# Performance work log

Hardware: AMD Instinct MI355X
Metric: run time of the kernel (lower is better)

The kernel has to match this reference:

```python
import jax, jax.numpy as jnp
import numpy as np

EMBED_DIM = 768
NUM_HEADS = 12
D_K = EMBED_DIM // NUM_HEADS


def setup_inputs() -> dict:
    key = jax.random.key(0)
    ks = jax.random.split(key, 9)
    b, s, d = 4, 2048, EMBED_DIM
    scale = 1.0 / np.sqrt(d)
    x = jax.random.normal(ks[0], (b, s, d), dtype=jnp.float32)
    return {
        "x": x,
        "w_q": jax.random.normal(ks[1], (d, d), dtype=jnp.float32) * scale,
        "b_q": jnp.zeros((d,), dtype=jnp.float32),
        "w_k": jax.random.normal(ks[2], (d, d), dtype=jnp.float32) * scale,
        "b_k": jnp.zeros((d,), dtype=jnp.float32),
        "w_v": jax.random.normal(ks[3], (d, d), dtype=jnp.float32) * scale,
        "b_v": jnp.zeros((d,), dtype=jnp.float32),
        "w_o": jax.random.normal(ks[4], (d, d), dtype=jnp.float32) * scale,
        "b_o": jnp.zeros((d,), dtype=jnp.float32),
    }


def reference(x, w_q, b_q, w_k, b_k, w_v, b_v, w_o, b_o):
    b, s, d = x.shape
    h, dk = NUM_HEADS, D_K
    # projections (torch Linear: x @ W^T + b)
    q = (x @ w_q.T + b_q).reshape(b, s, h, dk).transpose(0, 2, 1, 3)
    k = (x @ w_k.T + b_k).reshape(b, s, h, dk).transpose(0, 2, 1, 3)
    v = (x @ w_v.T + b_v).reshape(b, s, h, dk).transpose(0, 2, 1, 3)
    # causal attention: full [b,h,s,s] scores as in the original
    scores = jnp.einsum("bhqd,bhkd->bhqk", q, k) / jnp.sqrt(jnp.float32(dk))
    causal = jnp.tril(jnp.ones((s, s), dtype=bool))
    scores = jnp.where(causal[None, None], scores, -jnp.inf)
    attn = jax.nn.softmax(scores, axis=-1)
    out = jnp.einsum("bhqk,bhkd->bhqd", attn, v)
    out = out.transpose(0, 2, 1, 3).reshape(b, s, h * dk)
    return out @ w_o.T + b_o
```

## Files before the change

kernel.cpp:

```cpp
#include <hip/hip_runtime.h>
#include <hip/hip_bf16.h>
#include <stdint.h>

typedef short bf16x8 __attribute__((ext_vector_type(8)));
typedef float f32x4 __attribute__((ext_vector_type(4)));
typedef unsigned short u16;


__device__ __forceinline__ u16 f2bf_bits(float f) {
    __hip_bfloat16 h = __float2bfloat16(f);
    return __builtin_bit_cast(u16, h);
}

__device__ __forceinline__ uint32_t pack2bf(float a, float b) {
    uint32_t ua = __builtin_bit_cast(uint32_t, a) + 0x8000u;
    uint32_t ub = __builtin_bit_cast(uint32_t, b) + 0x8000u;
    return __builtin_amdgcn_perm(ub, ua, 0x07060302u);
}

__device__ __forceinline__ void gld_lds16(const void* g, void* l) {
    __builtin_amdgcn_global_load_lds(
        (const __attribute__((address_space(1))) void*)g,
        (__attribute__((address_space(3))) void*)l, 16, 0, 0);
}

#define CEXP 0.18033688011112042f


__global__ __launch_bounds__(256) void cast_x_kernel(const float* __restrict__ x,
                                                     u16* __restrict__ o, int n4) {
    int i = blockIdx.x * 256 + threadIdx.x;
    if (i >= n4) return;
    float4 v = ((const float4*)x)[i];
    ushort4 u;
    u.x = f2bf_bits(v.x); u.y = f2bf_bits(v.y);
    u.z = f2bf_bits(v.z); u.w = f2bf_bits(v.w);
    ((ushort4*)o)[i] = u;
}

__global__ __launch_bounds__(256) void cast_w_kernel(
    const float* __restrict__ w0, const float* __restrict__ w1,
    const float* __restrict__ w2, const float* __restrict__ w3,
    u16* __restrict__ o0, u16* __restrict__ o1,
    u16* __restrict__ o2, u16* __restrict__ o3,
    const float* __restrict__ bq, const float* __restrict__ bk,
    const float* __restrict__ bv, float* __restrict__ biasf) {
    int gid = blockIdx.x * 256 + threadIdx.x;
    int which = gid / 147456;
    int off = gid - which * 147456;
    const float* s = which == 0 ? w0 : which == 1 ? w1 : which == 2 ? w2 : w3;
    u16* d        = which == 0 ? o0 : which == 1 ? o1 : which == 2 ? o2 : o3;
    float4 v = ((const float4*)s)[off];
    ushort4 u;
    u.x = f2bf_bits(v.x); u.y = f2bf_bits(v.y);
    u.z = f2bf_bits(v.z); u.w = f2bf_bits(v.w);
    ((ushort4*)d)[off] = u;
    if (gid < 2304) {
        float bb = gid < 768 ? bq[gid] : gid < 1536 ? bk[gid - 768] : bv[gid - 1536];
        biasf[gid] = bb;
    }
}


template <int RT, int OUTF>
__global__ __launch_bounds__(256) void gemm_xwt(
    const u16* __restrict__ X, const u16* __restrict__ W,
    const float* __restrict__ bias, float* __restrict__ Cf,
    u16* __restrict__ Cb, int K, int NC) {
    constexpr int JR = RT / 32;
    __shared__ u16 lsX[RT * 32];
    __shared__ u16 lsW[128 * 32];
    const int tid = threadIdx.x;
    const int w = tid >> 6, lane = tid & 63;
    const int quad = lane >> 4, l15 = lane & 15;
    const int m0 = blockIdx.y * RT, n0 = blockIdx.x * 128;
    const int wr = (w >> 1) * (RT / 2), wc = (w & 1) * 64;
    const int r4 = lane >> 2, c4 = lane & 3;
    const int cglob = c4 ^ (((lane >> 2) ^ (lane >> 4)) & 3);

    f32x4 acc[JR][4];
    for (int j = 0; j < JR; ++j)
        for (int i = 0; i < 4; ++i) acc[j][i] = (f32x4){0.f, 0.f, 0.f, 0.f};

    const int KT = K / 32;
    for (int kt = 0; kt < KT; ++kt) {
        const int k0 = kt * 32;
        __syncthreads();
        {
            int row = w * 16 + r4;
            gld_lds16(X + (size_t)(m0 + row) * K + k0 + cglob * 8, &lsX[w * 512]);
            if (RT == 128)
                gld_lds16(X + (size_t)(m0 + 64 + row) * K + k0 + cglob * 8,
                          &lsX[(w + 4) * 512]);
            gld_lds16(W + (size_t)(n0 + row) * K + k0 + cglob * 8, &lsW[w * 512]);
            gld_lds16(W + (size_t)(n0 + 64 + row) * K + k0 + cglob * 8,
                      &lsW[(w + 4) * 512]);
        }
        __syncthreads();

        const int sl = (l15 ^ (l15 >> 2)) & 3;
        bf16x8 xf[JR], wf[4];
        for (int j = 0; j < JR; ++j) {
            int row = wr + j * 16 + l15;
            xf[j] = *(const bf16x8*)&lsX[row * 32 + ((quad ^ sl) & 3) * 8];
        }
        for (int i = 0; i < 4; ++i) {
            int row = wc + i * 16 + l15;
            wf[i] = *(const bf16x8*)&lsW[row * 32 + ((quad ^ sl) & 3) * 8];
        }
        for (int j = 0; j < JR; ++j)
            for (int i = 0; i < 4; ++i)
                acc[j][i] = __builtin_amdgcn_mfma_f32_16x16x32_bf16(wf[i], xf[j],
                                                                   acc[j][i], 0, 0, 0);
    }

    for (int i = 0; i < 4; ++i) {
        int c0 = n0 + wc + i * 16 + quad * 4;
        float4 bv4 = *(const float4*)&bias[c0];
        for (int j = 0; j < JR; ++j) {
            int row = m0 + wr + j * 16 + l15;
            float v0 = acc[j][i][0] + bv4.x;
            float v1 = acc[j][i][1] + bv4.y;
            float v2 = acc[j][i][2] + bv4.z;
            float v3 = acc[j][i][3] + bv4.w;
            if (OUTF) {
                float4 o4 = {v0, v1, v2, v3};
                *(float4*)&Cf[(size_t)row * NC + c0] = o4;
            } else {
                uint2 pk = {pack2bf(v0, v1), pack2bf(v2, v3)};
                *(uint2*)&Cb[(size_t)row * NC + c0] = pk;
            }
        }
    }
}


__global__ __launch_bounds__(256) void transpose_v(const u16* __restrict__ QKV,
                                                   u16* __restrict__ Vt) {
    __shared__ u16 t[64 * 66];
    int bx = blockIdx.x;
    int st = bx & 31, bh = bx >> 5;
    int b = bh / 12, h = bh % 12;
    int tid = threadIdx.x;
    int c = tid & 63, r4 = tid >> 6;
    for (int i = 0; i < 16; ++i) {
        int s = i * 4 + r4;
        t[s * 66 + c] = QKV[(size_t)(b * 2048 + st * 64 + s) * 2304 + 1536 + h * 64 + c];
    }
    __syncthreads();
    for (int i = 0; i < 16; ++i) {
        int d = i * 4 + r4;
        Vt[(size_t)(bh * 64 + d) * 2048 + st * 64 + c] = t[c * 66 + d];
    }
}


__global__ __launch_bounds__(256, 3) void attn_kernel(
    const u16* __restrict__ QKV, const u16* __restrict__ Vt, u16* __restrict__ O) {
    __shared__ u16 lsQ[128 * 64];
    __shared__ u16 lsK[64 * 64];
    __shared__ u16 lsV[64 * 64];
    __shared__ u16 lsP[4][32 * 72];

    int bx = blockIdx.x;
    int bh = bx % 48;
    int qtb = 15 - (bx / 48);
    int b = bh / 12, h = bh % 12;
    int tid = threadIdx.x, w = tid >> 6, lane = tid & 63;
    int quad = lane >> 4, l15 = lane & 15;
    int rr = lane >> 3, c8 = lane & 7;

    for (int cb = w; cb < 16; cb += 4) {
        int row = cb * 8 + rr;
        int cg = c8 ^ ((rr ^ cb) & 7);
        gld_lds16(QKV + (size_t)(b * 2048 + qtb * 128 + row) * 2304 + h * 64 + cg * 8,
                  &lsQ[cb * 512]);
    }
    __syncthreads();

    bf16x8 q0[2], q1[2];
    for (int g = 0; g < 2; ++g) {
        int rowq = g * 64 + w * 16 + l15;
        int swq = (rowq ^ (rowq >> 3)) & 7;
        q0[g] = *(const bf16x8*)&lsQ[rowq * 64 + ((0 + quad) ^ swq) * 8];
        q1[g] = *(const bf16x8*)&lsQ[rowq * 64 + ((4 + quad) ^ swq) * 8];
    }

    f32x4 oacc0[4], oacc1[4];
    for (int dt = 0; dt < 4; ++dt) {
        oacc0[dt] = (f32x4){0.f, 0.f, 0.f, 0.f};
        oacc1[dt] = (f32x4){0.f, 0.f, 0.f, 0.f};
    }
    float li0 = 0.f, li1 = 0.f;
    u16* Pw = lsP[w];
    const int qrel = w * 16 + l15;
    const int ktmax = 2 * qtb + 1;

    for (int kt = 0; kt <= ktmax; ++kt) {
        __syncthreads();
        for (int cb = w; cb < 8; cb += 4) {
            int row = cb * 8 + rr;
            int cg = c8 ^ ((rr ^ cb) & 7);
            gld_lds16(QKV + (size_t)(b * 2048 + kt * 64 + row) * 2304 + 768 + h * 64 + cg * 8,
                      &lsK[cb * 512]);
            gld_lds16(Vt + (size_t)(bh * 64 + row) * 2048 + kt * 64 + cg * 8,
                      &lsV[cb * 512]);
        }
        __syncthreads();

        const bool do0 = (kt <= 2 * qtb);

        f32x4 S0[4], S1[4];
        for (int ct = 0; ct < 4; ++ct) {
            int rowk = ct * 16 + l15;
            int swk = (rowk ^ (rowk >> 3)) & 7;
            bf16x8 k0 = *(const bf16x8*)&lsK[rowk * 64 + ((0 + quad) ^ swk) * 8];
            bf16x8 k1 = *(const bf16x8*)&lsK[rowk * 64 + ((4 + quad) ^ swk) * 8];
            f32x4 z = (f32x4){0.f, 0.f, 0.f, 0.f};
            S1[ct] = __builtin_amdgcn_mfma_f32_16x16x32_bf16(k0, q0[1], z, 0, 0, 0);
            S1[ct] = __builtin_amdgcn_mfma_f32_16x16x32_bf16(k1, q1[1], S1[ct], 0, 0, 0);
            if (do0) {
                S0[ct] = __builtin_amdgcn_mfma_f32_16x16x32_bf16(k0, q0[0], z, 0, 0, 0);
                S0[ct] = __builtin_amdgcn_mfma_f32_16x16x32_bf16(k1, q1[0], S0[ct], 0, 0, 0);
            }
        }

        if (kt == 2 * qtb) {
            for (int ct = 0; ct < 4; ++ct) {
                int kbase = ct * 16 + quad * 4;
                for (int r = 0; r < 4; ++r)
                    if (kbase + r > qrel) S0[ct][r] = -1e30f;
            }
        }
        if (kt == 2 * qtb + 1) {
            for (int ct = 0; ct < 4; ++ct) {
                int kbase = ct * 16 + quad * 4;
                for (int r = 0; r < 4; ++r)
                    if (kbase + r > qrel) S1[ct][r] = -1e30f;
            }
        }

        if (do0) {
            u16* Pr = &Pw[(size_t)l15 * 72];
            for (int ct = 0; ct < 4; ++ct) {
                float p0 = __builtin_amdgcn_exp2f(S0[ct][0] * CEXP);
                float p1 = __builtin_amdgcn_exp2f(S0[ct][1] * CEXP);
                float p2 = __builtin_amdgcn_exp2f(S0[ct][2] * CEXP);
                float p3 = __builtin_amdgcn_exp2f(S0[ct][3] * CEXP);
                li0 += (p0 + p1) + (p2 + p3);
                uint2 pk = {pack2bf(p0, p1), pack2bf(p2, p3)};
                *(uint2*)&Pr[ct * 16 + quad * 4] = pk;
            }
        }
        {
            u16* Pr = &Pw[(size_t)(16 + l15) * 72];
            for (int ct = 0; ct < 4; ++ct) {
                float p0 = __builtin_amdgcn_exp2f(S1[ct][0] * CEXP);
                float p1 = __builtin_amdgcn_exp2f(S1[ct][1] * CEXP);
                float p2 = __builtin_amdgcn_exp2f(S1[ct][2] * CEXP);
                float p3 = __builtin_amdgcn_exp2f(S1[ct][3] * CEXP);
                li1 += (p0 + p1) + (p2 + p3);
                uint2 pk = {pack2bf(p0, p1), pack2bf(p2, p3)};
                *(uint2*)&Pr[ct * 16 + quad * 4] = pk;
            }
        }

        for (int ks = 0; ks < 2; ++ks) {
            bf16x8 bp1 = *(const bf16x8*)&Pw[(size_t)(16 + l15) * 72 + ks * 32 + quad * 8];
            bf16x8 bp0;
            if (do0) bp0 = *(const bf16x8*)&Pw[(size_t)l15 * 72 + ks * 32 + quad * 8];
            for (int dt = 0; dt < 4; ++dt) {
                int rowv = dt * 16 + l15;
                int swv = (rowv ^ (rowv >> 3)) & 7;
                bf16x8 av = *(const bf16x8*)&lsV[rowv * 64 + ((ks * 4 + quad) ^ swv) * 8];
                oacc1[dt] = __builtin_amdgcn_mfma_f32_16x16x32_bf16(av, bp1, oacc1[dt], 0, 0, 0);
                if (do0)
                    oacc0[dt] = __builtin_amdgcn_mfma_f32_16x16x32_bf16(av, bp0, oacc0[dt], 0, 0, 0);
            }
        }
    }

    li0 += __shfl_xor(li0, 16, 64);
    li0 += __shfl_xor(li0, 32, 64);
    li1 += __shfl_xor(li1, 16, 64);
    li1 += __shfl_xor(li1, 32, 64);
    float inv0 = 1.0f / li0, inv1 = 1.0f / li1;

    for (int g = 0; g < 2; ++g) {
        float inv = g ? inv1 : inv0;
        f32x4* oa = g ? oacc1 : oacc0;
        int row = qtb * 128 + g * 64 + w * 16 + l15;
        for (int dt = 0; dt < 4; ++dt) {
            uint2 pk = {pack2bf(oa[dt][0] * inv, oa[dt][1] * inv),
                        pack2bf(oa[dt][2] * inv, oa[dt][3] * inv)};
            *(uint2*)&O[(size_t)(b * 2048 + row) * 768 + h * 64 + dt * 16 + quad * 4] = pk;
        }
    }
}


extern "C" void kernel_launch(void* const* d_in, const int* in_sizes, int n_in,
                              void* d_out, int out_size, void* d_ws, size_t ws_size,
                              hipStream_t stream) {
    const float* x  = (const float*)d_in[0];
    const float* wq = (const float*)d_in[1];
    const float* bq = (const float*)d_in[2];
    const float* wk = (const float*)d_in[3];
    const float* bk = (const float*)d_in[4];
    const float* wv = (const float*)d_in[5];
    const float* bv = (const float*)d_in[6];
    const float* wo = (const float*)d_in[7];
    const float* bo = (const float*)d_in[8];
    float* out = (float*)d_out;

    char* ws = (char*)d_ws;
    u16*   xb    = (u16*)(ws + 0);
    u16*   Wf    = (u16*)(ws + 12582912);
    u16*   wob   = (u16*)(ws + 16121856);
    float* biasf = (float*)(ws + 17301504);
    u16*   QKVb  = (u16*)(ws + 17310720);
    u16*   Vtw   = (u16*)(ws + 55059456);
    u16*   Ow    = (u16*)(ws + 67642368);

    cast_x_kernel<<<6144, 256, 0, stream>>>(x, xb, 1572864);
    cast_w_kernel<<<2304, 256, 0, stream>>>(wq, wk, wv, wo,
                                            Wf, Wf + 589824, Wf + 1179648, wob,
                                            bq, bk, bv, biasf);

    gemm_xwt<128, 0><<<dim3(18, 64), 256, 0, stream>>>(xb, Wf, biasf, nullptr, QKVb,
                                                       768, 2304);
    transpose_v<<<1536, 256, 0, stream>>>(QKVb, Vtw);
    attn_kernel<<<768, 256, 0, stream>>>(QKVb, Vtw, Ow);
    gemm_xwt<64, 1><<<dim3(6, 128), 256, 0, stream>>>(Ow, wob, bo, out, nullptr,
                                                      768, 768);
}
```

Baseline: 233.3 us.

## Fuse casts, write V transposed from QKV GEMM epilogue, deepen GEMM K-tile

Merges the x and weight cast kernels into one launch. Removes the separate V-transpose kernel: the QKV GEMM epilogue writes V columns straight into the transposed Vt layout. It also doubles the GEMM K-tile from 32 to 64 with a new 8-way XOR swizzle, halving the number of barrier and load rounds. The transposed epilogue uses scattered 2-byte stores instead of packed writes, and the larger LDS tile may reduce occupancy.

Result: faster. 215.3 us (-7.7%).

```diff
diff --git a/kernel.cpp b/kernel.cpp
--- a/kernel.cpp
+++ b/kernel.cpp
@@ -27,29 +27,27 @@
 #define CEXP 0.18033688011112042f
 
 
-__global__ __launch_bounds__(256) void cast_x_kernel(const float* __restrict__ x,
-                                                     u16* __restrict__ o, int n4) {
-    int i = blockIdx.x * 256 + threadIdx.x;
-    if (i >= n4) return;
-    float4 v = ((const float4*)x)[i];
-    ushort4 u;
-    u.x = f2bf_bits(v.x); u.y = f2bf_bits(v.y);
-    u.z = f2bf_bits(v.z); u.w = f2bf_bits(v.w);
-    ((ushort4*)o)[i] = u;
-}
-
-__global__ __launch_bounds__(256) void cast_w_kernel(
-    const float* __restrict__ w0, const float* __restrict__ w1,
-    const float* __restrict__ w2, const float* __restrict__ w3,
+__global__ __launch_bounds__(256) void cast_all_kernel(
+    const float* __restrict__ x, const float* __restrict__ w0,
+    const float* __restrict__ w1, const float* __restrict__ w2,
+    const float* __restrict__ w3, u16* __restrict__ xb,
     u16* __restrict__ o0, u16* __restrict__ o1,
     u16* __restrict__ o2, u16* __restrict__ o3,
     const float* __restrict__ bq, const float* __restrict__ bk,
     const float* __restrict__ bv, float* __restrict__ biasf) {
     int gid = blockIdx.x * 256 + threadIdx.x;
-    int which = gid / 147456;
-    int off = gid - which * 147456;
-    const float* s = which == 0 ? w0 : which == 1 ? w1 : which == 2 ? w2 : w3;
-    u16* d        = which == 0 ? o0 : which == 1 ? o1 : which == 2 ? o2 : o3;
+    const float* s;
+    u16* d;
+    int off;
+    if (gid < 1572864) {
+        s = x; d = xb; off = gid;
+    } else {
+        int g2 = gid - 1572864;
+        int which = g2 / 147456;
+        off = g2 - which * 147456;
+        s = which == 0 ? w0 : which == 1 ? w1 : which == 2 ? w2 : w3;
+        d = which == 0 ? o0 : which == 1 ? o1 : which == 2 ? o2 : o3;
+    }
     float4 v = ((const float4*)s)[off];
     ushort4 u;
     u.x = f2bf_bits(v.x); u.y = f2bf_bits(v.y);
@@ -62,58 +60,61 @@
 }
 
 
-template <int RT, int OUTF>
+template <int RT, int MODE>
 __global__ __launch_bounds__(256) void gemm_xwt(
     const u16* __restrict__ X, const u16* __restrict__ W,
     const float* __restrict__ bias, float* __restrict__ Cf,
-    u16* __restrict__ Cb, int K, int NC) {
+    u16* __restrict__ Cb, u16* __restrict__ Vt, int K, int NC) {
     constexpr int JR = RT / 32;
-    __shared__ u16 lsX[RT * 32];
-    __shared__ u16 lsW[128 * 32];
+    __shared__ u16 lsX[RT * 64];
+    __shared__ u16 lsW[128 * 64];
     const int tid = threadIdx.x;
     const int w = tid >> 6, lane = tid & 63;
     const int quad = lane >> 4, l15 = lane & 15;
     const int m0 = blockIdx.y * RT, n0 = blockIdx.x * 128;
     const int wr = (w >> 1) * (RT / 2), wc = (w & 1) * 64;
-    const int r4 = lane >> 2, c4 = lane & 3;
-    const int cglob = c4 ^ (((lane >> 2) ^ (lane >> 4)) & 3);
+    const int rr = lane >> 3, c8 = lane & 7;
 
     f32x4 acc[JR][4];
     for (int j = 0; j < JR; ++j)
         for (int i = 0; i < 4; ++i) acc[j][i] = (f32x4){0.f, 0.f, 0.f, 0.f};
 
-    const int KT = K / 32;
+    const int KT = K / 64;
     for (int kt = 0; kt < KT; ++kt) {
-        const int k0 = kt * 32;
+        const int k0 = kt * 64;
         __syncthreads();
-        {
-            int row = w * 16 + r4;
-            gld_lds16(X + (size_t)(m0 + row) * K + k0 + cglob * 8, &lsX[w * 512]);
-            if (RT == 128)
-                gld_lds16(X + (size_t)(m0 + 64 + row) * K + k0 + cglob * 8,
-                          &lsX[(w + 4) * 512]);
-            gld_lds16(W + (size_t)(n0 + row) * K + k0 + cglob * 8, &lsW[w * 512]);
-            gld_lds16(W + (size_t)(n0 + 64 + row) * K + k0 + cglob * 8,
-                      &lsW[(w + 4) * 512]);
+        for (int cb = w; cb < RT / 8; cb += 4) {
+            int row = cb * 8 + rr;
+            int cg = c8 ^ ((rr ^ cb) & 7);
+            gld_lds16(X + (size_t)(m0 + row) * K + k0 + cg * 8, &lsX[cb * 512]);
+        }
+        for (int cb = w; cb < 16; cb += 4) {
+            int row = cb * 8 + rr;
+            int cg = c8 ^ ((rr ^ cb) & 7);
+            gld_lds16(W + (size_t)(n0 + row) * K + k0 + cg * 8, &lsW[cb * 512]);
         }
         __syncthreads();
 
-        const int sl = (l15 ^ (l15 >> 2)) & 3;
-        bf16x8 xf[JR], wf[4];
-        for (int j = 0; j < JR; ++j) {
-            int row = wr + j * 16 + l15;
-            xf[j] = *(const bf16x8*)&lsX[row * 32 + ((quad ^ sl) & 3) * 8];
-        }
-        for (int i = 0; i < 4; ++i) {
-            int row = wc + i * 16 + l15;
-            wf[i] = *(const bf16x8*)&lsW[row * 32 + ((quad ^ sl) & 3) * 8];
-        }
-        for (int j = 0; j < JR; ++j)
-            for (int i = 0; i < 4; ++i)
-                acc[j][i] = __builtin_amdgcn_mfma_f32_16x16x32_bf16(wf[i], xf[j],
-                                                                   acc[j][i], 0, 0, 0);
-    }
-
+        for (int kk = 0; kk < 2; ++kk) {
+            bf16x8 xf[JR], wf[4];
+            for (int j = 0; j < JR; ++j) {
+                int row = wr + j * 16 + l15;
+                int slot = (kk * 4 + quad) ^ ((row ^ (row >> 3)) & 7);
+                xf[j] = *(const bf16x8*)&lsX[row * 64 + slot * 8];
+            }
+            for (int i = 0; i < 4; ++i) {
+                int row = wc + i * 16 + l15;
+                int slot = (kk * 4 + quad) ^ ((row ^ (row >> 3)) & 7);
+                wf[i] = *(const bf16x8*)&lsW[row * 64 + slot * 8];
+            }
+            for (int j = 0; j < JR; ++j)
+                for (int i = 0; i < 4; ++i)
+                    acc[j][i] = __builtin_amdgcn_mfma_f32_16x16x32_bf16(
+                        wf[i], xf[j], acc[j][i], 0, 0, 0);
+        }
+    }
+
+    const bool vtile = (MODE == 2) && (n0 >= 1536);
     for (int i = 0; i < 4; ++i) {
         int c0 = n0 + wc + i * 16 + quad * 4;
         float4 bv4 = *(const float4*)&bias[c0];
@@ -123,34 +124,24 @@
             float v1 = acc[j][i][1] + bv4.y;
             float v2 = acc[j][i][2] + bv4.z;
             float v3 = acc[j][i][3] + bv4.w;
-            if (OUTF) {
+            if (MODE == 1) {
                 float4 o4 = {v0, v1, v2, v3};
                 *(float4*)&Cf[(size_t)row * NC + c0] = o4;
+            } else if (vtile) {
+                int d = c0 - 1536;
+                int bq_ = row >> 11;
+                int s = row & 2047;
+                int h = d >> 6, dd = d & 63;
+                size_t base = ((size_t)(bq_ * 12 + h) * 64 + dd) * 2048 + s;
+                Vt[base]          = f2bf_bits(v0);
+                Vt[base + 2048]   = f2bf_bits(v1);
+                Vt[base + 4096]   = f2bf_bits(v2);
+                Vt[base + 6144]   = f2bf_bits(v3);
             } else {
                 uint2 pk = {pack2bf(v0, v1), pack2bf(v2, v3)};
                 *(uint2*)&Cb[(size_t)row * NC + c0] = pk;
             }
         }
-    }
-}
-
-
-__global__ __launch_bounds__(256) void transpose_v(const u16* __restrict__ QKV,
-                                                   u16* __restrict__ Vt) {
-    __shared__ u16 t[64 * 66];
-    int bx = blockIdx.x;
-    int st = bx & 31, bh = bx >> 5;
-    int b = bh / 12, h = bh % 12;
-    int tid = threadIdx.x;
-    int c = tid & 63, r4 = tid >> 6;
-    for (int i = 0; i < 16; ++i) {
-        int s = i * 4 + r4;
-        t[s * 66 + c] = QKV[(size_t)(b * 2048 + st * 64 + s) * 2304 + 1536 + h * 64 + c];
-    }
-    __syncthreads();
-    for (int i = 0; i < 16; ++i) {
-        int d = i * 4 + r4;
-        Vt[(size_t)(bh * 64 + d) * 2048 + st * 64 + c] = t[c * 66 + d];
     }
 }
 
@@ -322,15 +313,13 @@
     u16*   Vtw   = (u16*)(ws + 55059456);
     u16*   Ow    = (u16*)(ws + 67642368);
 
-    cast_x_kernel<<<6144, 256, 0, stream>>>(x, xb, 1572864);
-    cast_w_kernel<<<2304, 256, 0, stream>>>(wq, wk, wv, wo,
-                                            Wf, Wf + 589824, Wf + 1179648, wob,
-                                            bq, bk, bv, biasf);
-
-    gemm_xwt<128, 0><<<dim3(18, 64), 256, 0, stream>>>(xb, Wf, biasf, nullptr, QKVb,
-                                                       768, 2304);
-    transpose_v<<<1536, 256, 0, stream>>>(QKVb, Vtw);
+    cast_all_kernel<<<8448, 256, 0, stream>>>(x, wq, wk, wv, wo,
+                                              xb, Wf, Wf + 589824, Wf + 1179648, wob,
+                                              bq, bk, bv, biasf);
+
+    gemm_xwt<128, 2><<<dim3(18, 64), 256, 0, stream>>>(xb, Wf, biasf, nullptr, QKVb,
+                                                       Vtw, 768, 2304);
     attn_kernel<<<768, 256, 0, stream>>>(QKVb, Vtw, Ow);
     gemm_xwt<64, 1><<<dim3(6, 128), 256, 0, stream>>>(Ow, wob, bo, out, nullptr,
-                                                      768, 768);
-}
+                                                      nullptr, 768, 768);
+}
```
